# Kernel tuning notes

Hardware: AMD Instinct MI355X
Metric: run time of the kernel (lower is better)

## Reference

```python
import jax, jax.numpy as jnp
import numpy as np

B, L = 16384, 32
IN_DIM, TIME_DIM, HIDDEN, HEADS = 128, 64, 256, 4
HEAD_DIM = HIDDEN // HEADS
KV_DIM = IN_DIM + 2 * TIME_DIM
EPS = 1e-5


def setup_inputs() -> dict:
    key = jax.random.key(0)
    ks = jax.random.split(key, 16)
    s = lambda d: 1.0 / np.sqrt(d)
    return {
        "x_u": jax.random.normal(ks[0], (B, IN_DIM), jnp.float32),
        "x_ctx": jax.random.normal(ks[1], (B, L, IN_DIM), jnp.float32),
        "t_ctx": jax.random.uniform(ks[2], (B, L), jnp.float32) * 100.0,
        "freq": jax.random.normal(ks[3], (TIME_DIM,), jnp.float32),
        "phase": jnp.zeros((TIME_DIM,), jnp.float32),
        "Wq": jax.random.normal(ks[4], (IN_DIM, HIDDEN), jnp.float32) * s(IN_DIM),
        "Wk": jax.random.normal(ks[5], (KV_DIM, HIDDEN), jnp.float32) * s(KV_DIM),
        "Wv": jax.random.normal(ks[6], (KV_DIM, HIDDEN), jnp.float32) * s(KV_DIM),
        "Wres": jax.random.normal(ks[7], (IN_DIM, HIDDEN), jnp.float32) * s(IN_DIM),
        "bres": jnp.zeros((HIDDEN,), jnp.float32),
        "W1": jax.random.normal(ks[8], (HIDDEN, HIDDEN), jnp.float32) * s(HIDDEN),
        "b1": jnp.zeros((HIDDEN,), jnp.float32),
        "W2": jax.random.normal(ks[9], (HIDDEN, HIDDEN), jnp.float32) * s(HIDDEN),
        "b2": jnp.zeros((HIDDEN,), jnp.float32),
        "g1": jnp.ones((HIDDEN,), jnp.float32),
        "be1": jnp.zeros((HIDDEN,), jnp.float32),
        "g2": jnp.ones((HIDDEN,), jnp.float32),
        "be2": jnp.zeros((HIDDEN,), jnp.float32),
    }


def _layernorm(x, g, b):
    m = jnp.mean(x, axis=-1, keepdims=True)
    v = jnp.mean((x - m) ** 2, axis=-1, keepdims=True)
    return (x - m) * jax.lax.rsqrt(v + EPS) * g + b


def reference(x_u, x_ctx, t_ctx, freq, phase, Wq, Wk, Wv, Wres, bres,
              W1, b1, W2, b2, g1, be1, g2, be2):
    # --- time encoding: [B, L, 2*TIME_DIM]
    z = jnp.log1p(jnp.maximum(t_ctx, 0.0))[..., None] * freq + phase
    te = jnp.concatenate([jnp.sin(z), jnp.cos(z)], axis=-1)

    # --- single-query multi-head attention over L neighbors
    q = (x_u @ Wq).reshape(B, HEADS, HEAD_DIM)            # [B,H,d]
    kv = jnp.concatenate([x_ctx, te], axis=-1)            # [B,L,KV_DIM]
    k = (kv @ Wk).reshape(B, L, HEADS, HEAD_DIM)          # [B,L,H,d]
    v = (kv @ Wv).reshape(B, L, HEADS, HEAD_DIM)
    att = jnp.einsum('bhd,blhd->bhl', q, k) / np.sqrt(HEAD_DIM)
    att = jax.nn.softmax(att, axis=-1)                    # [B,H,L]
    agg = jnp.einsum('bhl,blhd->bhd', att, v).reshape(B, HIDDEN)

    # --- residual + norms + FFN (dropout is identity in eval)
    z1 = _layernorm(agg + x_u @ Wres + bres, g1, be1)
    ff = jax.nn.relu(z1 @ W1 + b1) @ W2 + b2
    return _layernorm(ff + z1, g2, be2)
```

## Files before the change

kernel.cpp:

```cpp
#include <hip/hip_runtime.h>

typedef unsigned short u16;
typedef unsigned int   u32;

using bf16x8 = __attribute__((ext_vector_type(8))) short;
using f32x4  = __attribute__((ext_vector_type(4))) float;

#define MFMA16(A, B, C) __builtin_amdgcn_mfma_f32_16x16x32_bf16((A), (B), (C), 0, 0, 0)

static __device__ __forceinline__ u16 f2b(float f) {
    u32 u = __builtin_bit_cast(u32, f);
    u32 r = (u + 0x7FFFu + ((u >> 16) & 1u)) >> 16;
    return (u16)r;
}
static __device__ __forceinline__ u16 f2bh(float f) {
    u32 u = __builtin_bit_cast(u32, f) + 0x8000u;
    return (u16)(u >> 16);
}
static __device__ __forceinline__ u32 pk2(float fa, float fb) {
    u32 a = __builtin_bit_cast(u32, fa) + 0x8000u;
    u32 b = __builtin_bit_cast(u32, fb) + 0x8000u;
    return __builtin_amdgcn_perm(b, a, 0x07060302u);
}
static __device__ __forceinline__ bf16x8 cvt8f(f32x4 a, f32x4 b) {
    union { u32 w[4]; bf16x8 v; } r;
    r.w[0] = pk2(a[0], a[1]); r.w[1] = pk2(a[2], a[3]);
    r.w[2] = pk2(b[0], b[1]); r.w[3] = pk2(b[2], b[3]);
    return r.v;
}
static __device__ __forceinline__ bf16x8 cvt8(f32x4 a, f32x4 b) {
    bf16x8 r;
    r[0] = (short)f2b(a[0]); r[1] = (short)f2b(a[1]);
    r[2] = (short)f2b(a[2]); r[3] = (short)f2b(a[3]);
    r[4] = (short)f2b(b[0]); r[5] = (short)f2b(b[1]);
    r[6] = (short)f2b(b[2]); r[7] = (short)f2b(b[3]);
    return r;
}

__global__ __launch_bounds__(256) void k0_prep(
    const float* __restrict__ Wq, const float* __restrict__ Wk,
    const float* __restrict__ Wv, const float* __restrict__ Wres,
    const float* __restrict__ W1, const float* __restrict__ W2,
    u16* __restrict__ WcatT, u16* __restrict__ WresT,
    u16* __restrict__ WvT, u16* __restrict__ W1T, u16* __restrict__ W2T)
{
    int t = blockIdx.x * 256 + threadIdx.x;
    if (t < 131072) {
        int n = t >> 7, i = t & 127;
        int h = n >> 8, c = n & 255;
        const float* wq = Wq + i * 256 + h * 64;
        const float* wk = Wk + c * 256 + h * 64;
        float acc = 0.f;
        #pragma unroll 8
        for (int d = 0; d < 64; ++d) acc += wq[d] * wk[d];
        WcatT[t] = f2b(acc * 0.125f);
    } else if (t < 163840) {
        int o = t - 131072; int n = o >> 7, i = o & 127;
        WresT[o] = f2b(Wres[i * 256 + n]);
    } else if (t < 229376) {
        int o = t - 163840; int n = o >> 8, c = o & 255;
        WvT[o] = f2b(Wv[c * 256 + n]);
    } else if (t < 294912) {
        int o = t - 229376; int n = o >> 8, c = o & 255;
        W1T[o] = f2b(W1[c * 256 + n]);
    } else {
        int o = t - 294912; int n = o >> 8, c = o & 255;
        W2T[o] = f2b(W2[c * 256 + n]);
    }
}

__global__ __launch_bounds__(256, 4) void kf_fused(
    const float* __restrict__ xu, const float* __restrict__ x_ctx,
    const float* __restrict__ t_ctx, const float* __restrict__ freq,
    const float* __restrict__ phase,
    const u16* __restrict__ WcatT, const u16* __restrict__ WvT,
    const u16* __restrict__ WresT, const u16* __restrict__ W1T,
    const u16* __restrict__ W2T,
    const float* __restrict__ bres, const float* __restrict__ b1,
    const float* __restrict__ b2, const float* __restrict__ g1,
    const float* __restrict__ be1, const float* __restrict__ g2,
    const float* __restrict__ be2, float* __restrict__ out)
{
    __shared__ __align__(16) char smem[40576];
    u16  (*kv)[1032]   = reinterpret_cast<u16 (*)[1032]>(smem);
    u16  (*xus)[136]   = reinterpret_cast<u16 (*)[136]>(smem + 33024);
    u16  (*pw)[4][32]  = reinterpret_cast<u16 (*)[4][32]>(smem + 37376);
    float(*red)[16][2] = reinterpret_cast<float (*)[16][2]>(smem + 38400);
    float(*mrstd)[2]   = reinterpret_cast<float (*)[2]>(smem + 40448);
    float(*zbuf)[264]  = reinterpret_cast<float (*)[264]>(smem);
    u16  (*z1b)[264]   = reinterpret_cast<u16 (*)[264]>(smem + 16896);
    u16  (*h1b)[264]   = reinterpret_cast<u16 (*)[264]>(smem + 25344);
    float(*obuf)[264]  = reinterpret_cast<float (*)[264]>(smem + 16896);

    const int b0 = blockIdx.x * 16;
    const int t = threadIdx.x;
    const int lane = t & 63, wave = t >> 6;
    const int quad = lane >> 4, l16 = lane & 15;
    const int fb = quad * 8;
    const int nw = wave * 64;
    const f32x4 zz = {0.f, 0.f, 0.f, 0.f};

    {
        int row = t >> 4, ch = t & 15;
        const float* src = xu + (size_t)(b0 + row) * 128 + ch * 8;
        *(bf16x8*)&xus[row][ch * 8] = cvt8(*(const f32x4*)src, *(const f32x4*)(src + 4));
    }
    __syncthreads();

    #pragma unroll 4
    for (int nt = 0; nt < 16; ++nt) {
        int n0 = wave * 256 + nt * 16;
        f32x4 acc = zz;
        #pragma unroll
        for (int ks = 0; ks < 4; ++ks) {
            bf16x8 afr = *(const bf16x8*)&xus[l16][ks * 32 + fb];
            bf16x8 bfr = *(const bf16x8*)(WcatT + (size_t)(n0 + l16) * 128 + ks * 32 + fb);
            acc = MFMA16(afr, bfr, acc);
        }
        #pragma unroll
        for (int r = 0; r < 4; ++r)
            kv[quad * 4 + r][n0 + l16] = f2b(acc[r]);
    }
    __syncthreads();

    f32x4 fr0a = *(const f32x4*)(freq + fb);
    f32x4 fr0b = *(const f32x4*)(freq + fb + 4);
    f32x4 fr1a = *(const f32x4*)(freq + 32 + fb);
    f32x4 fr1b = *(const f32x4*)(freq + 32 + fb + 4);
    f32x4 ph0a = *(const f32x4*)(phase + fb);
    f32x4 ph0b = *(const f32x4*)(phase + fb + 4);
    f32x4 ph1a = *(const f32x4*)(phase + 32 + fb);
    f32x4 ph1b = *(const f32x4*)(phase + 32 + fb + 4);

    for (int i = 0; i < 4; ++i) {
        const int kvrow = wave * 4 + i;
        const int b = b0 + kvrow;
        float ltv = log1pf(fmaxf(t_ctx[(size_t)b * 32 + (lane & 31)], 0.f));
        const u16* qb = &kv[kvrow][(l16 & 3) * 256];

        f32x4 accA[2];
        #pragma unroll
        for (int ltile = 0; ltile < 2; ++ltile) {
            const int l = ltile * 16 + l16;
            const float* xrow = x_ctx + ((size_t)b * 32 + l) * 128;
            f32x4 acc = zz;
            #pragma unroll
            for (int ks = 0; ks < 4; ++ks) {
                f32x4 a = *(const f32x4*)(xrow + ks * 32 + fb);
                f32x4 c = *(const f32x4*)(xrow + ks * 32 + fb + 4);
                acc = MFMA16(cvt8f(a, c), *(const bf16x8*)(qb + ks * 32 + fb), acc);
            }
            float lt_l = __shfl(ltv, l);
            f32x4 z0a = fr0a * lt_l + ph0a;
            f32x4 z0b = fr0b * lt_l + ph0b;
            f32x4 z1a = fr1a * lt_l + ph1a;
            f32x4 z1b_ = fr1b * lt_l + ph1b;
            f32x4 s0a, s0b, s1a, s1b, c0a, c0b, c1a, c1b;
            #pragma unroll
            for (int j = 0; j < 4; ++j) {
                s0a[j] = __sinf(z0a[j]); s0b[j] = __sinf(z0b[j]);
                s1a[j] = __sinf(z1a[j]); s1b[j] = __sinf(z1b_[j]);
                c0a[j] = __cosf(z0a[j]); c0b[j] = __cosf(z0b[j]);
                c1a[j] = __cosf(z1a[j]); c1b[j] = __cosf(z1b_[j]);
            }
            acc = MFMA16(cvt8f(s0a, s0b), *(const bf16x8*)(qb + 128 + fb), acc);
            acc = MFMA16(cvt8f(s1a, s1b), *(const bf16x8*)(qb + 160 + fb), acc);
            acc = MFMA16(cvt8f(c0a, c0b), *(const bf16x8*)(qb + 192 + fb), acc);
            acc = MFMA16(cvt8f(c1a, c1b), *(const bf16x8*)(qb + 224 + fb), acc);
            accA[ltile] = acc;
        }

        float m = accA[0][0];
        #pragma unroll
        for (int r = 1; r < 4; ++r) m = fmaxf(m, accA[0][r]);
        #pragma unroll
        for (int r = 0; r < 4; ++r) m = fmaxf(m, accA[1][r]);
        m = fmaxf(m, __shfl_xor(m, 16));
        m = fmaxf(m, __shfl_xor(m, 32));
        float p[2][4], s = 0.f;
        #pragma unroll
        for (int lt2 = 0; lt2 < 2; ++lt2)
            #pragma unroll
            for (int r = 0; r < 4; ++r) { p[lt2][r] = __expf(accA[lt2][r] - m); s += p[lt2][r]; }
        s += __shfl_xor(s, 16);
        s += __shfl_xor(s, 32);
        float inv = 1.f / s;
        if (l16 < 4) {
            #pragma unroll
            for (int lt2 = 0; lt2 < 2; ++lt2)
                #pragma unroll
                for (int r = 0; r < 4; ++r)
                    pw[wave][l16][lt2 * 16 + quad * 4 + r] = f2bh(p[lt2][r] * inv);
        }
        __syncthreads();

        bf16x8 pfr = *(const bf16x8*)&pw[wave][l16 & 3][fb];
        float ltj[8];
        #pragma unroll
        for (int j = 0; j < 8; ++j) ltj[j] = __shfl(ltv, fb + j);

        #pragma unroll
        for (int nt = 0; nt < 8; ++nt) {
            int c = nt * 16 + l16;
            const float* xp = x_ctx + ((size_t)b * 32 + fb) * 128 + c;
            float v0 = xp[0], v1 = xp[128], v2 = xp[256], v3 = xp[384];
            float v4 = xp[512], v5 = xp[640], v6 = xp[768], v7 = xp[896];
            union { u32 w[4]; bf16x8 v; } bu;
            bu.w[0] = pk2(v0, v1); bu.w[1] = pk2(v2, v3);
            bu.w[2] = pk2(v4, v5); bu.w[3] = pk2(v6, v7);
            f32x4 d = MFMA16(pfr, bu.v, zz);
            if (quad == 0) {
                #pragma unroll
                for (int r = 0; r < 4; ++r) kv[kvrow][r * 256 + c] = f2bh(d[r]);
            }
        }
        #pragma unroll
        for (int pp = 0; pp < 4; ++pp) {
            int f = pp * 16 + l16;
            float fq = freq[f], phf = phase[f];
            float z8[8];
            #pragma unroll
            for (int j = 0; j < 8; ++j) z8[j] = ltj[j] * fq + phf;
            union { u32 w[4]; bf16x8 v; } bs, bc;
            #pragma unroll
            for (int j = 0; j < 4; ++j) {
                bs.w[j] = pk2(__sinf(z8[2 * j]), __sinf(z8[2 * j + 1]));
                bc.w[j] = pk2(__cosf(z8[2 * j]), __cosf(z8[2 * j + 1]));
            }
            f32x4 ds = MFMA16(pfr, bs.v, zz);
            f32x4 dc = MFMA16(pfr, bc.v, zz);
            if (quad == 0) {
                #pragma unroll
                for (int r = 0; r < 4; ++r) {
                    kv[kvrow][r * 256 + 128 + f] = f2bh(ds[r]);
                    kv[kvrow][r * 256 + 192 + f] = f2bh(dc[r]);
                }
            }
        }
    }
    __syncthreads();

    f32x4 acc[4];
    #pragma unroll
    for (int nt = 0; nt < 4; ++nt) acc[nt] = zz;
    #pragma unroll
    for (int ks = 0; ks < 8; ++ks) {
        bf16x8 afr = *(const bf16x8*)&kv[l16][wave * 256 + ks * 32 + quad * 8];
        #pragma unroll
        for (int nt = 0; nt < 4; ++nt) {
            bf16x8 bfr = *(const bf16x8*)(WvT + (size_t)(nw + nt * 16 + l16) * 256 + ks * 32 + quad * 8);
            acc[nt] = MFMA16(afr, bfr, acc[nt]);
        }
    }
    #pragma unroll
    for (int ks = 0; ks < 4; ++ks) {
        bf16x8 afr = *(const bf16x8*)&xus[l16][ks * 32 + quad * 8];
        #pragma unroll
        for (int nt = 0; nt < 4; ++nt) {
            bf16x8 bfr = *(const bf16x8*)(WresT + (size_t)(nw + nt * 16 + l16) * 128 + ks * 32 + quad * 8);
            acc[nt] = MFMA16(afr, bfr, acc[nt]);
        }
    }
    __syncthreads();
    #pragma unroll
    for (int nt = 0; nt < 4; ++nt) {
        int col = nw + nt * 16 + l16;
        float bb = bres[col];
        #pragma unroll
        for (int r = 0; r < 4; ++r)
            zbuf[quad * 4 + r][col] = acc[nt][r] + bb;
    }
    __syncthreads();

    {
        int row = t >> 4, j = t & 15;
        float s = 0.f, s2 = 0.f;
        #pragma unroll
        for (int i2 = 0; i2 < 16; ++i2) { float v = zbuf[row][j + 16 * i2]; s += v; s2 += v * v; }
        red[row][j][0] = s; red[row][j][1] = s2;
    }
    __syncthreads();
    if (t < 16) {
        float s = 0.f, s2 = 0.f;
        #pragma unroll
        for (int j = 0; j < 16; ++j) { s += red[t][j][0]; s2 += red[t][j][1]; }
        float m = s * (1.f / 256.f);
        float var = s2 * (1.f / 256.f) - m * m;
        mrstd[t][0] = m;
        mrstd[t][1] = rsqrtf(var + 1e-5f);
    }
    __syncthreads();
    {
        float g = g1[t], be = be1[t];
        #pragma unroll
        for (int i2 = 0; i2 < 16; ++i2) {
            float z = (zbuf[i2][t] - mrstd[i2][0]) * mrstd[i2][1] * g + be;
            zbuf[i2][t] = z;
            z1b[i2][t] = f2b(z);
        }
    }
    __syncthreads();

    f32x4 acc2[4];
    #pragma unroll
    for (int nt = 0; nt < 4; ++nt) acc2[nt] = zz;
    #pragma unroll
    for (int ks = 0; ks < 8; ++ks) {
        bf16x8 afr = *(const bf16x8*)&z1b[l16][ks * 32 + quad * 8];
        #pragma unroll
        for (int nt = 0; nt < 4; ++nt) {
            bf16x8 bfr = *(const bf16x8*)(W1T + (size_t)(nw + nt * 16 + l16) * 256 + ks * 32 + quad * 8);
            acc2[nt] = MFMA16(afr, bfr, acc2[nt]);
        }
    }
    #pragma unroll
    for (int nt = 0; nt < 4; ++nt) {
        int col = nw + nt * 16 + l16;
        float bb = b1[col];
        #pragma unroll
        for (int r = 0; r < 4; ++r)
            h1b[quad * 4 + r][col] = f2b(fmaxf(acc2[nt][r] + bb, 0.f));
    }
    __syncthreads();

    f32x4 acc3[4];
    #pragma unroll
    for (int nt = 0; nt < 4; ++nt) acc3[nt] = zz;
    #pragma unroll
    for (int ks = 0; ks < 8; ++ks) {
        bf16x8 afr = *(const bf16x8*)&h1b[l16][ks * 32 + quad * 8];
        #pragma unroll
        for (int nt = 0; nt < 4; ++nt) {
            bf16x8 bfr = *(const bf16x8*)(W2T + (size_t)(nw + nt * 16 + l16) * 256 + ks * 32 + quad * 8);
            acc3[nt] = MFMA16(afr, bfr, acc3[nt]);
        }
    }
    __syncthreads();
    #pragma unroll
    for (int nt = 0; nt < 4; ++nt) {
        int col = nw + nt * 16 + l16;
        float bb = b2[col];
        #pragma unroll
        for (int r = 0; r < 4; ++r) {
            int row = quad * 4 + r;
            obuf[row][col] = acc3[nt][r] + bb + zbuf[row][col];
        }
    }
    __syncthreads();

    {
        int row = t >> 4, j = t & 15;
        float s = 0.f, s2 = 0.f;
        #pragma unroll
        for (int i2 = 0; i2 < 16; ++i2) { float v = obuf[row][j + 16 * i2]; s += v; s2 += v * v; }
        red[row][j][0] = s; red[row][j][1] = s2;
    }
    __syncthreads();
    if (t < 16) {
        float s = 0.f, s2 = 0.f;
        #pragma unroll
        for (int j = 0; j < 16; ++j) { s += red[t][j][0]; s2 += red[t][j][1]; }
        float m = s * (1.f / 256.f);
        float var = s2 * (1.f / 256.f) - m * m;
        mrstd[t][0] = m;
        mrstd[t][1] = rsqrtf(var + 1e-5f);
    }
    __syncthreads();
    {
        float g = g2[t], be = be2[t];
        #pragma unroll
        for (int i2 = 0; i2 < 16; ++i2)
            out[(size_t)(b0 + i2) * 256 + t] = (obuf[i2][t] - mrstd[i2][0]) * mrstd[i2][1] * g + be;
    }
}

extern "C" void kernel_launch(void* const* d_in, const int* in_sizes, int n_in,
                              void* d_out, int out_size, void* d_ws, size_t ws_size,
                              hipStream_t stream)
{
    (void)in_sizes; (void)n_in; (void)out_size; (void)ws_size;
    const float* xu    = (const float*)d_in[0];
    const float* x_ctx = (const float*)d_in[1];
    const float* t_ctx = (const float*)d_in[2];
    const float* freq  = (const float*)d_in[3];
    const float* phase = (const float*)d_in[4];
    const float* Wq    = (const float*)d_in[5];
    const float* Wk    = (const float*)d_in[6];
    const float* Wv    = (const float*)d_in[7];
    const float* Wres  = (const float*)d_in[8];
    const float* bres  = (const float*)d_in[9];
    const float* W1    = (const float*)d_in[10];
    const float* b1    = (const float*)d_in[11];
    const float* W2    = (const float*)d_in[12];
    const float* b2    = (const float*)d_in[13];
    const float* g1    = (const float*)d_in[14];
    const float* be1   = (const float*)d_in[15];
    const float* g2    = (const float*)d_in[16];
    const float* be2   = (const float*)d_in[17];
    float* out = (float*)d_out;

    char* ws = (char*)d_ws;
    u16* WcatT = (u16*)(ws);
    u16* WresT = (u16*)(ws + 262144);
    u16* WvT   = (u16*)(ws + 327680);
    u16* W1T   = (u16*)(ws + 458752);
    u16* W2T   = (u16*)(ws + 589824);

    hipLaunchKernelGGL(k0_prep, dim3(1408), dim3(256), 0, stream,
                       Wq, Wk, Wv, Wres, W1, W2, WcatT, WresT, WvT, W1T, W2T);
    hipLaunchKernelGGL(kf_fused, dim3(1024), dim3(256), 0, stream,
                       xu, x_ctx, t_ctx, freq, phase,
                       WcatT, WvT, WresT, W1T, W2T,
                       bres, b1, b2, g1, be1, g2, be2, out);
}
```

Baseline: 499.4 us.

## Double block size to eight waves and split per-wave attention and GEMM work

Launches the fused kernel with 512 threads per block, 16 rows each, instead of 256. The attention rows, the q·Wk projection tiles and the Wv/Wres/W1/W2 output columns are all split across eight waves instead of four. It also drops the block-wide barrier inside the attention loop, since the probability scratch is wave-private. The aim is more waves in flight to hide the global-load latency of x_ctx and the weights. The tighter launch bound (512, 8) cuts the register budget and risks spills, and the per-row LayerNorm reductions now leave half the threads idle.

Result: slower. 555.3 us (+11.2%).

```diff
diff --git a/kernel.cpp b/kernel.cpp
--- a/kernel.cpp
+++ b/kernel.cpp
@@ -69,7 +69,7 @@
     }
 }
 
-__global__ __launch_bounds__(256, 4) void kf_fused(
+__global__ __launch_bounds__(512, 8) void kf_fused(
     const float* __restrict__ xu, const float* __restrict__ x_ctx,
     const float* __restrict__ t_ctx, const float* __restrict__ freq,
     const float* __restrict__ phase,
@@ -81,12 +81,12 @@
     const float* __restrict__ be1, const float* __restrict__ g2,
     const float* __restrict__ be2, float* __restrict__ out)
 {
-    __shared__ __align__(16) char smem[40576];
+    __shared__ __align__(16) char smem[39552];
     u16  (*kv)[1032]   = reinterpret_cast<u16 (*)[1032]>(smem);
     u16  (*xus)[136]   = reinterpret_cast<u16 (*)[136]>(smem + 33024);
     u16  (*pw)[4][32]  = reinterpret_cast<u16 (*)[4][32]>(smem + 37376);
-    float(*red)[16][2] = reinterpret_cast<float (*)[16][2]>(smem + 38400);
-    float(*mrstd)[2]   = reinterpret_cast<float (*)[2]>(smem + 40448);
+    float(*red)[16][2] = reinterpret_cast<float (*)[16][2]>(smem + 37376);
+    float(*mrstd)[2]   = reinterpret_cast<float (*)[2]>(smem + 39424);
     float(*zbuf)[264]  = reinterpret_cast<float (*)[264]>(smem);
     u16  (*z1b)[264]   = reinterpret_cast<u16 (*)[264]>(smem + 16896);
     u16  (*h1b)[264]   = reinterpret_cast<u16 (*)[264]>(smem + 25344);
@@ -97,10 +97,9 @@
     const int lane = t & 63, wave = t >> 6;
     const int quad = lane >> 4, l16 = lane & 15;
     const int fb = quad * 8;
-    const int nw = wave * 64;
     const f32x4 zz = {0.f, 0.f, 0.f, 0.f};
 
-    {
+    if (t < 256) {
         int row = t >> 4, ch = t & 15;
         const float* src = xu + (size_t)(b0 + row) * 128 + ch * 8;
         *(bf16x8*)&xus[row][ch * 8] = cvt8(*(const f32x4*)src, *(const f32x4*)(src + 4));
@@ -108,8 +107,8 @@
     __syncthreads();
 
     #pragma unroll 4
-    for (int nt = 0; nt < 16; ++nt) {
-        int n0 = wave * 256 + nt * 16;
+    for (int nt = 0; nt < 8; ++nt) {
+        int n0 = wave * 128 + nt * 16;
         f32x4 acc = zz;
         #pragma unroll
         for (int ks = 0; ks < 4; ++ks) {
@@ -132,17 +131,18 @@
     f32x4 ph1a = *(const f32x4*)(phase + 32 + fb);
     f32x4 ph1b = *(const f32x4*)(phase + 32 + fb + 4);
 
-    for (int i = 0; i < 4; ++i) {
-        const int kvrow = wave * 4 + i;
+    for (int i = 0; i < 2; ++i) {
+        const int kvrow = wave * 2 + i;
         const int b = b0 + kvrow;
         float ltv = log1pf(fmaxf(t_ctx[(size_t)b * 32 + (lane & 31)], 0.f));
         const u16* qb = &kv[kvrow][(l16 & 3) * 256];
+        float lt_0 = __shfl(ltv, l16);
+        float lt_1 = __shfl(ltv, 16 + l16);
 
         f32x4 accA[2];
         #pragma unroll
         for (int ltile = 0; ltile < 2; ++ltile) {
-            const int l = ltile * 16 + l16;
-            const float* xrow = x_ctx + ((size_t)b * 32 + l) * 128;
+            const float* xrow = x_ctx + ((size_t)b * 32 + ltile * 16 + l16) * 128;
             f32x4 acc = zz;
             #pragma unroll
             for (int ks = 0; ks < 4; ++ks) {
@@ -150,7 +150,7 @@
                 f32x4 c = *(const f32x4*)(xrow + ks * 32 + fb + 4);
                 acc = MFMA16(cvt8f(a, c), *(const bf16x8*)(qb + ks * 32 + fb), acc);
             }
-            float lt_l = __shfl(ltv, l);
+            float lt_l = ltile ? lt_1 : lt_0;
             f32x4 z0a = fr0a * lt_l + ph0a;
             f32x4 z0b = fr0b * lt_l + ph0b;
             f32x4 z1a = fr1a * lt_l + ph1a;
@@ -170,6 +170,10 @@
             accA[ltile] = acc;
         }
 
+        float ltj[8];
+        #pragma unroll
+        for (int j = 0; j < 8; ++j) ltj[j] = __shfl(ltv, fb + j);
+
         float m = accA[0][0];
         #pragma unroll
         for (int r = 1; r < 4; ++r) m = fmaxf(m, accA[0][r]);
@@ -192,12 +196,8 @@
                 for (int r = 0; r < 4; ++r)
                     pw[wave][l16][lt2 * 16 + quad * 4 + r] = f2bh(p[lt2][r] * inv);
         }
-        __syncthreads();
 
         bf16x8 pfr = *(const bf16x8*)&pw[wave][l16 & 3][fb];
-        float ltj[8];
-        #pragma unroll
-        for (int j = 0; j < 8; ++j) ltj[j] = __shfl(ltv, fb + j);
 
         #pragma unroll
         for (int nt = 0; nt < 8; ++nt) {
@@ -240,14 +240,17 @@
     }
     __syncthreads();
 
-    f32x4 acc[4];
-    #pragma unroll
-    for (int nt = 0; nt < 4; ++nt) acc[nt] = zz;
+    const int nw = wave * 32;
+    const int hd = (wave >> 1) * 256;
+
+    f32x4 acc[2];
+    #pragma unroll
+    for (int nt = 0; nt < 2; ++nt) acc[nt] = zz;
     #pragma unroll
     for (int ks = 0; ks < 8; ++ks) {
-        bf16x8 afr = *(const bf16x8*)&kv[l16][wave * 256 + ks * 32 + quad * 8];
-        #pragma unroll
-        for (int nt = 0; nt < 4; ++nt) {
+        bf16x8 afr = *(const bf16x8*)&kv[l16][hd + ks * 32 + quad * 8];
+        #pragma unroll
+        for (int nt = 0; nt < 2; ++nt) {
             bf16x8 bfr = *(const bf16x8*)(WvT + (size_t)(nw + nt * 16 + l16) * 256 + ks * 32 + quad * 8);
             acc[nt] = MFMA16(afr, bfr, acc[nt]);
         }
@@ -256,14 +259,14 @@
     for (int ks = 0; ks < 4; ++ks) {
         bf16x8 afr = *(const bf16x8*)&xus[l16][ks * 32 + quad * 8];
         #pragma unroll
-        for (int nt = 0; nt < 4; ++nt) {
+        for (int nt = 0; nt < 2; ++nt) {
             bf16x8 bfr = *(const bf16x8*)(WresT + (size_t)(nw + nt * 16 + l16) * 128 + ks * 32 + quad * 8);
             acc[nt] = MFMA16(afr, bfr, acc[nt]);
         }
     }
     __syncthreads();
     #pragma unroll
-    for (int nt = 0; nt < 4; ++nt) {
+    for (int nt = 0; nt < 2; ++nt) {
         int col = nw + nt * 16 + l16;
         float bb = bres[col];
         #pragma unroll
@@ -272,7 +275,7 @@
     }
     __syncthreads();
 
-    {
+    if (t < 256) {
         int row = t >> 4, j = t & 15;
         float s = 0.f, s2 = 0.f;
         #pragma unroll
@@ -291,30 +294,32 @@
     }
     __syncthreads();
     {
-        float g = g1[t], be = be1[t];
-        #pragma unroll
-        for (int i2 = 0; i2 < 16; ++i2) {
-            float z = (zbuf[i2][t] - mrstd[i2][0]) * mrstd[i2][1] * g + be;
-            zbuf[i2][t] = z;
-            z1b[i2][t] = f2b(z);
-        }
-    }
-    __syncthreads();
-
-    f32x4 acc2[4];
-    #pragma unroll
-    for (int nt = 0; nt < 4; ++nt) acc2[nt] = zz;
+        int col = t & 255, rh = (t >> 8) * 8;
+        float g = g1[col], be = be1[col];
+        #pragma unroll
+        for (int i2 = 0; i2 < 8; ++i2) {
+            int row = rh + i2;
+            float z = (zbuf[row][col] - mrstd[row][0]) * mrstd[row][1] * g + be;
+            zbuf[row][col] = z;
+            z1b[row][col] = f2b(z);
+        }
+    }
+    __syncthreads();
+
+    f32x4 acc2[2];
+    #pragma unroll
+    for (int nt = 0; nt < 2; ++nt) acc2[nt] = zz;
     #pragma unroll
     for (int ks = 0; ks < 8; ++ks) {
         bf16x8 afr = *(const bf16x8*)&z1b[l16][ks * 32 + quad * 8];
         #pragma unroll
-        for (int nt = 0; nt < 4; ++nt) {
+        for (int nt = 0; nt < 2; ++nt) {
             bf16x8 bfr = *(const bf16x8*)(W1T + (size_t)(nw + nt * 16 + l16) * 256 + ks * 32 + quad * 8);
             acc2[nt] = MFMA16(afr, bfr, acc2[nt]);
         }
     }
     #pragma unroll
-    for (int nt = 0; nt < 4; ++nt) {
+    for (int nt = 0; nt < 2; ++nt) {
         int col = nw + nt * 16 + l16;
         float bb = b1[col];
         #pragma unroll
@@ -323,21 +328,21 @@
     }
     __syncthreads();
 
-    f32x4 acc3[4];
-    #pragma unroll
-    for (int nt = 0; nt < 4; ++nt) acc3[nt] = zz;
+    f32x4 acc3[2];
+    #pragma unroll
+    for (int nt = 0; nt < 2; ++nt) acc3[nt] = zz;
     #pragma unroll
     for (int ks = 0; ks < 8; ++ks) {
         bf16x8 afr = *(const bf16x8*)&h1b[l16][ks * 32 + quad * 8];
         #pragma unroll
-        for (int nt = 0; nt < 4; ++nt) {
+        for (int nt = 0; nt < 2; ++nt) {
             bf16x8 bfr = *(const bf16x8*)(W2T + (size_t)(nw + nt * 16 + l16) * 256 + ks * 32 + quad * 8);
             acc3[nt] = MFMA16(afr, bfr, acc3[nt]);
         }
     }
     __syncthreads();
     #pragma unroll
-    for (int nt = 0; nt < 4; ++nt) {
+    for (int nt = 0; nt < 2; ++nt) {
         int col = nw + nt * 16 + l16;
         float bb = b2[col];
         #pragma unroll
@@ -348,7 +353,7 @@
     }
     __syncthreads();
 
-    {
+    if (t < 256) {
         int row = t >> 4, j = t & 15;
         float s = 0.f, s2 = 0.f;
         #pragma unroll
@@ -367,10 +372,14 @@
     }
     __syncthreads();
     {
-        float g = g2[t], be = be2[t];
-        #pragma unroll
-        for (int i2 = 0; i2 < 16; ++i2)
-            out[(size_t)(b0 + i2) * 256 + t] = (obuf[i2][t] - mrstd[i2][0]) * mrstd[i2][1] * g + be;
+        int col = t & 255, rh = (t >> 8) * 8;
+        float g = g2[col], be = be2[col];
+        #pragma unroll
+        for (int i2 = 0; i2 < 8; ++i2) {
+            int row = rh + i2;
+            out[(size_t)(b0 + row) * 256 + col] =
+                (obuf[row][col] - mrstd[row][0]) * mrstd[row][1] * g + be;
+        }
     }
 }
 
@@ -408,7 +417,7 @@
 
     hipLaunchKernelGGL(k0_prep, dim3(1408), dim3(256), 0, stream,
                        Wq, Wk, Wv, Wres, W1, W2, WcatT, WresT, WvT, W1T, W2T);
-    hipLaunchKernelGGL(kf_fused, dim3(1024), dim3(256), 0, stream,
+    hipLaunchKernelGGL(kf_fused, dim3(1024), dim3(512), 0, stream,
                        xu, x_ctx, t_ctx, freq, phase,
                        WcatT, WvT, WresT, W1T, W2T,
                        bres, b1, b2, g1, be1, g2, be2, out);
```
